# Kernel tuning notes

Hardware: AMD Instinct MI355X
Metric: run time of the kernel (lower is better)

The kernel has to match this reference:

```python
import jax, jax.numpy as jnp
import numpy as np

B, NDOC, L, E = 32, 4, 512, 512
SCALE = np.float32(1.0 / np.sqrt(E))
NEG_INF = np.float32(-1e9)


def setup_inputs() -> dict:
    key = jax.random.key(0)
    k1, k2, k3, k4, k5, k6 = jax.random.split(key, 6)
    return {
        "x1": jax.random.normal(k1, (B, L, E), dtype=jnp.float32),
        "x2": jax.random.normal(k2, (B, NDOC, L, E), dtype=jnp.float32),
        "x1_len": jax.random.randint(k3, (B,), 0, L, dtype=jnp.int64),
        "x2_len": jax.random.randint(k4, (B, NDOC), 0, L, dtype=jnp.int64),
        "fusion_w": jax.random.normal(k5, (2 * E, E), dtype=jnp.float32) * 0.02,
        "fusion_b": jnp.zeros((E,), dtype=jnp.float32),
        "out_w": jax.random.normal(k6, (8 * E, 2 * E), dtype=jnp.float32) * 0.02,
        "out_b": jnp.zeros((2 * E,), dtype=jnp.float32),
    }


def reference(x1, x2, x1_len, x2_len, fusion_w, fusion_b, out_w, out_b):
    # Faithful to torch .repeat(1,4,...): concatenate 4 full copies along batch,
    # so attention row i pairs x1[i % B] with x2[i // 4, i % 4].
    x1_rep = jnp.tile(x1, (NDOC, 1, 1))          # [4B, L, E]
    x2_r = x2.reshape(-1, L, E)                  # [4B, L, E]

    x1_len_r = jnp.tile(x1_len, NDOC)            # [4B] (same tiling as x1_rep)
    x2_len_r = x2_len.reshape(-1)                # [4B]
    pos = jnp.arange(L)
    q_mask = pos[None, :] < x1_len_r[:, None]    # [4B, L]
    k_mask = pos[None, :] < x2_len_r[:, None]    # [4B, L]
    mask = q_mask[:, :, None] & k_mask[:, None, :]  # [4B, L, L]

    # scaled-dot-product attention with masked_fill(mask==0, -1e9)
    scores = jnp.einsum('bqe,bke->bqk', x1_rep, x2_r) * SCALE  # [4B, L, L]
    scores = jnp.where(mask, scores, NEG_INF)
    attn = jax.nn.softmax(scores, axis=-1)
    x1_att = jnp.einsum('bqk,bke->bqe', attn, x2_r)            # [4B, L, E]

    cat = jnp.concatenate([x1_rep - x1_att, x1_rep * x1_att], axis=-1)  # [4B, L, 2E]
    fus = jax.nn.relu(cat @ fusion_w + fusion_b)                        # [4B, L, E]

    x1_mean = jnp.mean(fus, axis=1)              # [4B, E]
    x1_max = jnp.max(fus, axis=1)                # [4B, E]
    pooled = jnp.concatenate([x1_mean.reshape(B, -1), x1_max.reshape(B, -1)], axis=-1)  # [B, 8E]
    out = jax.nn.relu(pooled @ out_w + out_b)    # [B, 2E]
    return out, attn
```

## Files before the change

### kernel.cpp

```cpp
#include <hip/hip_runtime.h>
#include <cstddef>

#define BATCH 32
#define NB    128
#define LL    512
#define EE    512
#define SCALE 0.044194173824159216f
#define NEG_INF -1e9f

typedef __attribute__((ext_vector_type(4))) float f32x4;
typedef __attribute__((ext_vector_type(8))) short s16x8;
typedef __attribute__((ext_vector_type(4))) unsigned short u16x4;

__device__ __forceinline__ unsigned short f2b(float f) {
    unsigned u = __float_as_uint(f);
    u += 0x7FFFu + ((u >> 16) & 1u);
    return (unsigned short)(u >> 16);
}
__device__ __forceinline__ float b2f(unsigned short h) {
    return __uint_as_float(((unsigned)h) << 16);
}

__device__ __forceinline__ void gld_lds16(const unsigned short* g, unsigned short* l) {
    __builtin_amdgcn_global_load_lds(
        (const __attribute__((address_space(1))) void*)g,
        (__attribute__((address_space(3))) void*)l, 16, 0, 0);
}

__global__ __launch_bounds__(256) void k_cvt_x1(
    const float* __restrict__ x1, unsigned short* __restrict__ x1bf)
{
    const size_t idx = (size_t)blockIdx.x * 256 + threadIdx.x;
    f32x4 v = *(const f32x4*)(x1 + idx * 4);
    u16x4 o = { f2b(v[0]), f2b(v[1]), f2b(v[2]), f2b(v[3]) };
    *(u16x4*)(x1bf + idx * 4) = o;
}

__global__ __launch_bounds__(256) void k_cvt_x2(
    const float* __restrict__ x2,
    unsigned short* __restrict__ x2bf, unsigned short* __restrict__ x2t)
{
    __shared__ float T[64][65];
    const int i = blockIdx.z, kb = blockIdx.y * 64, eb = blockIdx.x * 64;
    const float* src = x2 + (size_t)i * LL * EE;
    unsigned short* db = x2bf + (size_t)i * LL * EE;
    unsigned short* dt = x2t  + (size_t)i * LL * EE;
    const int t = threadIdx.x, r16 = t >> 4, c4 = (t & 15) * 4;
#pragma unroll
    for (int p = 0; p < 4; ++p) {
        int row = p * 16 + r16;
        f32x4 v = *(const f32x4*)(src + (size_t)(kb + row) * EE + eb + c4);
        T[row][c4] = v[0]; T[row][c4+1] = v[1]; T[row][c4+2] = v[2]; T[row][c4+3] = v[3];
        u16x4 o = { f2b(v[0]), f2b(v[1]), f2b(v[2]), f2b(v[3]) };
        *(u16x4*)(db + (size_t)(kb + row) * EE + eb + c4) = o;
    }
    __syncthreads();
#pragma unroll
    for (int p = 0; p < 4; ++p) {
        int erow = p * 16 + r16;
        u16x4 o = { f2b(T[c4][erow]), f2b(T[c4+1][erow]),
                    f2b(T[c4+2][erow]), f2b(T[c4+3][erow]) };
        *(u16x4*)(dt + (size_t)(eb + erow) * LL + kb + c4) = o;
    }
}

__global__ __launch_bounds__(256) void k_cvt_fw(
    const float* __restrict__ fw, unsigned short* __restrict__ fwt)
{
    __shared__ float T[64][65];
    const int jb = blockIdx.y * 64, eb = blockIdx.x * 64;
    const int t = threadIdx.x, r16 = t >> 4, c4 = (t & 15) * 4;
#pragma unroll
    for (int p = 0; p < 4; ++p) {
        int row = p * 16 + r16;
        f32x4 v = *(const f32x4*)(fw + (size_t)(jb + row) * EE + eb + c4);
        T[row][c4] = v[0]; T[row][c4+1] = v[1]; T[row][c4+2] = v[2]; T[row][c4+3] = v[3];
    }
    __syncthreads();
#pragma unroll
    for (int p = 0; p < 4; ++p) {
        int erow = p * 16 + r16;
#pragma unroll
        for (int k = 0; k < 4; ++k) {
            int jold = jb + c4 + k;
            int jn = (jold < 512) ? (2 * jold) : (2 * (jold - 512) + 1);
            fwt[(size_t)(eb + erow) * 1024 + jn] = f2b(T[c4 + k][erow]);
        }
    }
}

__global__ __launch_bounds__(1024, 4) void k_attn(
    const unsigned short* __restrict__ x1bf,
    const unsigned short* __restrict__ x2bf,
    const unsigned short* __restrict__ x2t,
    const int* __restrict__ x1_len, const int* __restrict__ x2_len,
    float* __restrict__ attn, unsigned short* __restrict__ Cbuf)
{
    __shared__ __align__(16) char smem[147456];
    unsigned short* Ast = (unsigned short*)smem;
    unsigned short* Bst = (unsigned short*)(smem + 8192);
    unsigned short* Bpv = (unsigned short*)(smem + 131072);
    float* rowred = (float*)(smem + 131072);
    float* rowst  = (float*)(smem + 131072 + 4096);

    const int i  = blockIdx.x;
    const int q0 = blockIdx.y * 128;
    const unsigned short* Ag = x1bf + (size_t)(i & 31) * LL * EE;
    const unsigned short* Bg = x2bf + (size_t)i * LL * EE;
    const unsigned short* Vg = x2t  + (size_t)i * LL * EE;
    const int t = threadIdx.x, lane = t & 63;
    const int w = t >> 6;
    const int m = lane & 15, quad = lane >> 4;
    const int lrow = lane >> 2, lcol = (lane & 3) * 8;
    const int wrow = w >> 3, wcol = w & 7;

    f32x4 acc[4][4];
#pragma unroll
    for (int r = 0; r < 4; ++r)
#pragma unroll
        for (int c = 0; c < 4; ++c) acc[r][c] = (f32x4){0.f, 0.f, 0.f, 0.f};

    for (int e0 = 0; e0 < EE; e0 += 32) {
        if (w < 8)
            gld_lds16(Ag + (size_t)(q0 + w * 16 + lrow) * EE + e0 + lcol, &Ast[w * 512]);
        gld_lds16(Bg + (size_t)((2 * w) * 16 + lrow) * EE + e0 + lcol, &Bst[(2 * w) * 512]);
        gld_lds16(Bg + (size_t)((2 * w + 1) * 16 + lrow) * EE + e0 + lcol, &Bst[(2 * w + 1) * 512]);
        __syncthreads();
        s16x8 af[4], bfr[4];
#pragma unroll
        for (int rt = 0; rt < 4; ++rt)
            af[rt] = *(const s16x8*)&Ast[(wrow * 64 + rt * 16 + m) * 32 + quad * 8];
#pragma unroll
        for (int ct = 0; ct < 4; ++ct)
            bfr[ct] = *(const s16x8*)&Bst[(wcol * 64 + ct * 16 + m) * 32 + quad * 8];
#pragma unroll
        for (int rt = 0; rt < 4; ++rt)
#pragma unroll
            for (int ct = 0; ct < 4; ++ct)
                acc[rt][ct] = __builtin_amdgcn_mfma_f32_16x16x32_bf16(
                    af[rt], bfr[ct], acc[rt][ct], 0, 0, 0);
        __syncthreads();
    }

    const int qlen = x1_len[i & 31];
    const int klen = x2_len[i];

#pragma unroll
    for (int rt = 0; rt < 4; ++rt)
#pragma unroll
        for (int reg = 0; reg < 4; ++reg) {
            const int l = q0 + wrow * 64 + rt * 16 + quad * 4 + reg;
            const bool qok = l < qlen;
#pragma unroll
            for (int ct = 0; ct < 4; ++ct) {
                const int k = wcol * 64 + ct * 16 + m;
                acc[rt][ct][reg] = (qok && k < klen) ? acc[rt][ct][reg] * SCALE : NEG_INF;
            }
        }

#pragma unroll
    for (int rt = 0; rt < 4; ++rt)
#pragma unroll
        for (int reg = 0; reg < 4; ++reg) {
            float v = fmaxf(fmaxf(acc[rt][0][reg], acc[rt][1][reg]),
                            fmaxf(acc[rt][2][reg], acc[rt][3][reg]));
            v = fmaxf(v, __shfl_xor(v, 1));
            v = fmaxf(v, __shfl_xor(v, 2));
            v = fmaxf(v, __shfl_xor(v, 4));
            v = fmaxf(v, __shfl_xor(v, 8));
            if (m == 0)
                rowred[wcol * 128 + wrow * 64 + rt * 16 + quad * 4 + reg] = v;
        }
    __syncthreads();
    if (t < 128) {
        float mx = rowred[t];
#pragma unroll
        for (int c = 1; c < 8; ++c) mx = fmaxf(mx, rowred[c * 128 + t]);
        rowst[t] = mx;
    }
    __syncthreads();

#pragma unroll
    for (int rt = 0; rt < 4; ++rt)
#pragma unroll
        for (int reg = 0; reg < 4; ++reg) {
            const int lloc = wrow * 64 + rt * 16 + quad * 4 + reg;
            const float mx = rowst[lloc];
            float s = 0.f;
#pragma unroll
            for (int ct = 0; ct < 4; ++ct) {
                float p = __expf(acc[rt][ct][reg] - mx);
                acc[rt][ct][reg] = p;
                s += p;
            }
            s += __shfl_xor(s, 1);
            s += __shfl_xor(s, 2);
            s += __shfl_xor(s, 4);
            s += __shfl_xor(s, 8);
            if (m == 0) rowred[wcol * 128 + lloc] = s;
        }
    __syncthreads();
    if (t < 128) {
        float s = 0.f;
#pragma unroll
        for (int c = 0; c < 8; ++c) s += rowred[c * 128 + t];
        rowst[t] = 1.0f / s;
    }
    __syncthreads();

    float* op = attn + (size_t)i * LL * LL;
#pragma unroll
    for (int rt = 0; rt < 4; ++rt)
#pragma unroll
        for (int reg = 0; reg < 4; ++reg) {
            const int lloc = wrow * 64 + rt * 16 + quad * 4 + reg;
            const float inv = rowst[lloc];
#pragma unroll
            for (int ct = 0; ct < 4; ++ct) {
                const int k = wcol * 64 + ct * 16 + m;
                float p = acc[rt][ct][reg] * inv;
                op[(size_t)(q0 + lloc) * LL + k] = p;
                unsigned off = (unsigned)(lloc * 1024 + k * 2) ^ (unsigned)((lloc & 7) << 4);
                *(unsigned short*)(smem + off) = f2b(p);
            }
        }
    __syncthreads();

    const int pwr = w >> 2, pwc = w & 3;
    unsigned short* Cb = Cbuf + (size_t)i * LL * 1024;
#pragma unroll
    for (int eh = 0; eh < 2; ++eh) {
        f32x4 acc2[2][4];
#pragma unroll
        for (int r = 0; r < 2; ++r)
#pragma unroll
            for (int c = 0; c < 4; ++c) acc2[r][c] = (f32x4){0.f, 0.f, 0.f, 0.f};

        for (int k0 = 0; k0 < LL; k0 += 32) {
            gld_lds16(Vg + (size_t)(eh * 256 + w * 16 + lrow) * LL + k0 + lcol, &Bpv[w * 512]);
            __syncthreads();
            s16x8 paf[2], pbf[4];
#pragma unroll
            for (int rt = 0; rt < 2; ++rt) {
                const int lr = pwr * 32 + rt * 16 + m;
                unsigned off = (unsigned)(lr * 1024 + (k0 + quad * 8) * 2)
                               ^ (unsigned)((lr & 7) << 4);
                paf[rt] = *(const s16x8*)(smem + off);
            }
#pragma unroll
            for (int ct = 0; ct < 4; ++ct)
                pbf[ct] = *(const s16x8*)&Bpv[(pwc * 64 + ct * 16 + m) * 32 + quad * 8];
#pragma unroll
            for (int rt = 0; rt < 2; ++rt)
#pragma unroll
                for (int ct = 0; ct < 4; ++ct)
                    acc2[rt][ct] = __builtin_amdgcn_mfma_f32_16x16x32_bf16(
                        paf[rt], pbf[ct], acc2[rt][ct], 0, 0, 0);
            __syncthreads();
        }

#pragma unroll
        for (int rt = 0; rt < 2; ++rt)
#pragma unroll
            for (int reg = 0; reg < 4; ++reg) {
                const int l = q0 + pwr * 32 + rt * 16 + quad * 4 + reg;
#pragma unroll
                for (int ct = 0; ct < 4; ++ct) {
                    const int e = eh * 256 + pwc * 64 + ct * 16 + m;
                    float att = acc2[rt][ct][reg];
                    float xv  = b2f(Ag[(size_t)l * EE + e]);
                    unsigned pr = (unsigned)f2b(xv - att) | ((unsigned)f2b(xv * att) << 16);
                    *(unsigned*)(Cb + (size_t)l * 1024 + 2 * e) = pr;
                }
            }
    }
}

__global__ __launch_bounds__(256) void k_fuse_mfma(
    const unsigned short* __restrict__ Cbuf,
    const unsigned short* __restrict__ fwt,
    const float* __restrict__ fb,
    float* __restrict__ pmean, float* __restrict__ pmax)
{
    __shared__ unsigned short Al[128 * 32];
    __shared__ unsigned short Bl[128 * 32];
    __shared__ float psum[2][128];
    __shared__ float pmx[2][128];
    const int i  = blockIdx.x;
    const int lt = blockIdx.y >> 2;
    const int e0 = (blockIdx.y & 3) * 128;
    const unsigned short* Ab = Cbuf + ((size_t)i * LL + lt * 128) * 1024;
    const int t = threadIdx.x, lane = t & 63;
    const int w = t >> 6, wrow = w >> 1, wcol = w & 1;
    const int m = lane & 15, quad = lane >> 4;
    const int lrow = lane >> 2, lcol = (lane & 3) * 8;

    float bias[4];
#pragma unroll
    for (int ct = 0; ct < 4; ++ct) bias[ct] = fb[e0 + wcol * 64 + ct * 16 + m];
    float csum[4] = {0.f, 0.f, 0.f, 0.f};
    float cmax[4] = {-3e38f, -3e38f, -3e38f, -3e38f};

    f32x4 acc[4][4];
#pragma unroll
    for (int r = 0; r < 4; ++r)
#pragma unroll
        for (int c = 0; c < 4; ++c) acc[r][c] = (f32x4){0.f, 0.f, 0.f, 0.f};

    for (int j0 = 0; j0 < 1024; j0 += 32) {
#pragma unroll
        for (int c = 0; c < 2; ++c) {
            const int s = c * 4 + w;
            gld_lds16(Ab + (size_t)(s * 16 + lrow) * 1024 + j0 + lcol, &Al[s * 512]);
            gld_lds16(fwt + (size_t)(e0 + s * 16 + lrow) * 1024 + j0 + lcol, &Bl[s * 512]);
        }
        __syncthreads();
        s16x8 af[4], bfr[4];
#pragma unroll
        for (int rt = 0; rt < 4; ++rt)
            af[rt] = *(const s16x8*)&Al[(wrow * 64 + rt * 16 + m) * 32 + quad * 8];
#pragma unroll
        for (int ct = 0; ct < 4; ++ct)
            bfr[ct] = *(const s16x8*)&Bl[(wcol * 64 + ct * 16 + m) * 32 + quad * 8];
#pragma unroll
        for (int rt = 0; rt < 4; ++rt)
#pragma unroll
            for (int ct = 0; ct < 4; ++ct)
                acc[rt][ct] = __builtin_amdgcn_mfma_f32_16x16x32_bf16(
                    af[rt], bfr[ct], acc[rt][ct], 0, 0, 0);
        __syncthreads();
    }
#pragma unroll
    for (int rt = 0; rt < 4; ++rt)
#pragma unroll
        for (int reg = 0; reg < 4; ++reg)
#pragma unroll
            for (int ct = 0; ct < 4; ++ct) {
                float f = fmaxf(acc[rt][ct][reg] + bias[ct], 0.f);
                csum[ct] += f;
                cmax[ct] = fmaxf(cmax[ct], f);
            }
#pragma unroll
    for (int ct = 0; ct < 4; ++ct) {
        csum[ct] += __shfl_xor(csum[ct], 16);
        csum[ct] += __shfl_xor(csum[ct], 32);
        cmax[ct] = fmaxf(cmax[ct], __shfl_xor(cmax[ct], 16));
        cmax[ct] = fmaxf(cmax[ct], __shfl_xor(cmax[ct], 32));
    }
    if (quad == 0) {
#pragma unroll
        for (int ct = 0; ct < 4; ++ct) {
            psum[wrow][wcol * 64 + ct * 16 + m] = csum[ct];
            pmx[wrow][wcol * 64 + ct * 16 + m] = cmax[ct];
        }
    }
    __syncthreads();
    if (t < 128) {
        float s  = psum[0][t] + psum[1][t];
        float mx = fmaxf(pmx[0][t], pmx[1][t]);
        pmean[((size_t)i * 4 + lt) * EE + e0 + t] = s;
        pmax[((size_t)i * 4 + lt) * EE + e0 + t]  = mx;
    }
}

__global__ __launch_bounds__(256) void k_out_split(
    const float* __restrict__ pmean, const float* __restrict__ pmax,
    const float* __restrict__ ow, float* __restrict__ partial)
{
    __shared__ float ps[256];
    const int kc = blockIdx.x;
    const int b  = blockIdx.y;
    const int t  = threadIdx.x;
    const int j  = kc * 256 + t;
    const int jj = (j < 2048) ? j : j - 2048;
    const int ii = 4 * b + (jj >> 9);
    const int e  = jj & 511;
    float v;
    if (j < 2048) {
        const float* bp = pmean + (size_t)ii * 4 * EE + e;
        v = (bp[0] + bp[512] + bp[1024] + bp[1536]) * (1.0f / 512.0f);
    } else {
        const float* bp = pmax + (size_t)ii * 4 * EE + e;
        v = fmaxf(fmaxf(bp[0], bp[512]), fmaxf(bp[1024], bp[1536]));
    }
    ps[t] = v;
    __syncthreads();
    f32x4 acc = {0.f, 0.f, 0.f, 0.f};
    const float* wp = ow + (size_t)kc * 256 * 1024 + t * 4;
#pragma unroll 8
    for (int q = 0; q < 256; ++q) {
        f32x4 w4 = *(const f32x4*)(wp + (size_t)q * 1024);
        float p = ps[q];
        acc[0] = fmaf(p, w4[0], acc[0]);
        acc[1] = fmaf(p, w4[1], acc[1]);
        acc[2] = fmaf(p, w4[2], acc[2]);
        acc[3] = fmaf(p, w4[3], acc[3]);
    }
    *(f32x4*)(partial + ((size_t)kc * 32 + b) * 1024 + t * 4) = acc;
}

__global__ __launch_bounds__(256) void k_out_final(
    const float* __restrict__ partial, const float* __restrict__ ob,
    float* __restrict__ out)
{
    const int idx = blockIdx.x * 256 + threadIdx.x;
    const int b = idx >> 10, o = idx & 1023;
    float s = ob[o];
#pragma unroll
    for (int kc = 0; kc < 16; ++kc)
        s += partial[((size_t)kc * 32 + b) * 1024 + o];
    out[idx] = fmaxf(s, 0.f);
}

extern "C" void kernel_launch(void* const* d_in, const int* in_sizes, int n_in,
                              void* d_out, int out_size, void* d_ws, size_t ws_size,
                              hipStream_t stream)
{
    const float* x1     = (const float*)d_in[0];
    const float* x2     = (const float*)d_in[1];
    const int*   x1_len = (const int*)d_in[2];
    const int*   x2_len = (const int*)d_in[3];
    const float* fw     = (const float*)d_in[4];
    const float* fb     = (const float*)d_in[5];
    const float* ow     = (const float*)d_in[6];
    const float* ob     = (const float*)d_in[7];

    float* out  = (float*)d_out;
    float* attn = out + (size_t)BATCH * 1024;

    char* wp = (char*)d_ws;
    unsigned short* x1bf   = (unsigned short*)wp; wp += (size_t)BATCH * LL * EE * 2;
    unsigned short* x2bf   = (unsigned short*)wp; wp += (size_t)NB * LL * EE * 2;
    unsigned short* x2t    = (unsigned short*)wp; wp += (size_t)NB * LL * EE * 2;
    unsigned short* Cbuf   = (unsigned short*)wp; wp += (size_t)NB * LL * 1024 * 2;
    unsigned short* fwt    = (unsigned short*)wp; wp += (size_t)EE * 1024 * 2;
    float* pmean   = (float*)wp; wp += (size_t)NB * 4 * EE * 4;
    float* pmax    = (float*)wp; wp += (size_t)NB * 4 * EE * 4;
    float* partial = (float*)wp; wp += (size_t)16 * BATCH * 1024 * 4;

    k_cvt_x1<<<dim3(BATCH * LL * EE / 4 / 256), 256, 0, stream>>>(x1, x1bf);
    k_cvt_x2<<<dim3(8, 8, NB), 256, 0, stream>>>(x2, x2bf, x2t);
    k_cvt_fw<<<dim3(8, 16), 256, 0, stream>>>(fw, fwt);
    k_attn<<<dim3(128, 4), 1024, 0, stream>>>(x1bf, x2bf, x2t, x1_len, x2_len, attn, Cbuf);
    k_fuse_mfma<<<dim3(128, 16), 256, 0, stream>>>(Cbuf, fwt, fb, pmean, pmax);
    k_out_split<<<dim3(16, BATCH), 256, 0, stream>>>(pmean, pmax, ow, partial);
    k_out_final<<<dim3(BATCH * 1024 / 256), 256, 0, stream>>>(partial, ob, out);
}
```

Measured before the change: 578.5 us.

## Double-buffer LDS staging in attention and fusion GEMM loops

Adds ping-pong LDS buffers to the QK^T, PV and fusion GEMM main loops. Each loop prefetches the next 32-wide K slice while MFMAs run on the current one, and drops one barrier per iteration. The aim is to hide global-to-LDS load latency behind matrix math. The cost is that the attention kernel's shared memory grows to 160 KB, the full per-CU LDS, and the fusion kernel's LDS use doubles, which may reduce occupancy there.

```diff
diff --git a/kernel.cpp b/kernel.cpp
--- a/kernel.cpp
+++ b/kernel.cpp
@@ -96,10 +96,13 @@
     const int* __restrict__ x1_len, const int* __restrict__ x2_len,
     float* __restrict__ attn, unsigned short* __restrict__ Cbuf)
 {
-    __shared__ __align__(16) char smem[147456];
-    unsigned short* Ast = (unsigned short*)smem;
-    unsigned short* Bst = (unsigned short*)(smem + 8192);
-    unsigned short* Bpv = (unsigned short*)(smem + 131072);
+    __shared__ __align__(16) char smem[163840];
+    unsigned short* A0 = (unsigned short*)smem;
+    unsigned short* B0 = (unsigned short*)(smem + 8192);
+    unsigned short* A1 = (unsigned short*)(smem + 40960);
+    unsigned short* B1 = (unsigned short*)(smem + 49152);
+    unsigned short* V0 = (unsigned short*)(smem + 131072);
+    unsigned short* V1 = (unsigned short*)(smem + 147456);
     float* rowred = (float*)(smem + 131072);
     float* rowst  = (float*)(smem + 131072 + 4096);
 
@@ -120,19 +123,31 @@
 #pragma unroll
         for (int c = 0; c < 4; ++c) acc[r][c] = (f32x4){0.f, 0.f, 0.f, 0.f};
 
-    for (int e0 = 0; e0 < EE; e0 += 32) {
-        if (w < 8)
-            gld_lds16(Ag + (size_t)(q0 + w * 16 + lrow) * EE + e0 + lcol, &Ast[w * 512]);
-        gld_lds16(Bg + (size_t)((2 * w) * 16 + lrow) * EE + e0 + lcol, &Bst[(2 * w) * 512]);
-        gld_lds16(Bg + (size_t)((2 * w + 1) * 16 + lrow) * EE + e0 + lcol, &Bst[(2 * w + 1) * 512]);
-        __syncthreads();
+    if (w < 8)
+        gld_lds16(Ag + (size_t)(q0 + w * 16 + lrow) * EE + lcol, &A0[w * 512]);
+    gld_lds16(Bg + (size_t)((2 * w) * 16 + lrow) * EE + lcol, &B0[(2 * w) * 512]);
+    gld_lds16(Bg + (size_t)((2 * w + 1) * 16 + lrow) * EE + lcol, &B0[(2 * w + 1) * 512]);
+    __syncthreads();
+
+    for (int it = 0; it < 16; ++it) {
+        unsigned short* Ac = (it & 1) ? A1 : A0;
+        unsigned short* Bc = (it & 1) ? B1 : B0;
+        if (it < 15) {
+            unsigned short* An = (it & 1) ? A0 : A1;
+            unsigned short* Bn = (it & 1) ? B0 : B1;
+            const int e0n = (it + 1) * 32;
+            if (w < 8)
+                gld_lds16(Ag + (size_t)(q0 + w * 16 + lrow) * EE + e0n + lcol, &An[w * 512]);
+            gld_lds16(Bg + (size_t)((2 * w) * 16 + lrow) * EE + e0n + lcol, &Bn[(2 * w) * 512]);
+            gld_lds16(Bg + (size_t)((2 * w + 1) * 16 + lrow) * EE + e0n + lcol, &Bn[(2 * w + 1) * 512]);
+        }
         s16x8 af[4], bfr[4];
 #pragma unroll
         for (int rt = 0; rt < 4; ++rt)
-            af[rt] = *(const s16x8*)&Ast[(wrow * 64 + rt * 16 + m) * 32 + quad * 8];
+            af[rt] = *(const s16x8*)&Ac[(wrow * 64 + rt * 16 + m) * 32 + quad * 8];
 #pragma unroll
         for (int ct = 0; ct < 4; ++ct)
-            bfr[ct] = *(const s16x8*)&Bst[(wcol * 64 + ct * 16 + m) * 32 + quad * 8];
+            bfr[ct] = *(const s16x8*)&Bc[(wcol * 64 + ct * 16 + m) * 32 + quad * 8];
 #pragma unroll
         for (int rt = 0; rt < 4; ++rt)
 #pragma unroll
@@ -236,9 +251,17 @@
 #pragma unroll
             for (int c = 0; c < 4; ++c) acc2[r][c] = (f32x4){0.f, 0.f, 0.f, 0.f};
 
-        for (int k0 = 0; k0 < LL; k0 += 32) {
-            gld_lds16(Vg + (size_t)(eh * 256 + w * 16 + lrow) * LL + k0 + lcol, &Bpv[w * 512]);
-            __syncthreads();
+        gld_lds16(Vg + (size_t)(eh * 256 + w * 16 + lrow) * LL + lcol, &V0[w * 512]);
+        __syncthreads();
+
+        for (int kt = 0; kt < 16; ++kt) {
+            const int k0 = kt * 32;
+            unsigned short* Vc = (kt & 1) ? V1 : V0;
+            if (kt < 15) {
+                unsigned short* Vn = (kt & 1) ? V0 : V1;
+                gld_lds16(Vg + (size_t)(eh * 256 + w * 16 + lrow) * LL + k0 + 32 + lcol,
+                          &Vn[w * 512]);
+            }
             s16x8 paf[2], pbf[4];
 #pragma unroll
             for (int rt = 0; rt < 2; ++rt) {
@@ -249,7 +272,7 @@
             }
 #pragma unroll
             for (int ct = 0; ct < 4; ++ct)
-                pbf[ct] = *(const s16x8*)&Bpv[(pwc * 64 + ct * 16 + m) * 32 + quad * 8];
+                pbf[ct] = *(const s16x8*)&Vc[(pwc * 64 + ct * 16 + m) * 32 + quad * 8];
 #pragma unroll
             for (int rt = 0; rt < 2; ++rt)
 #pragma unroll
@@ -282,8 +305,8 @@
     const float* __restrict__ fb,
     float* __restrict__ pmean, float* __restrict__ pmax)
 {
-    __shared__ unsigned short Al[128 * 32];
-    __shared__ unsigned short Bl[128 * 32];
+    __shared__ unsigned short Al[2][128 * 32];
+    __shared__ unsigned short Bl[2][128 * 32];
     __shared__ float psum[2][128];
     __shared__ float pmx[2][128];
     const int i  = blockIdx.x;
@@ -307,21 +330,34 @@
 #pragma unroll
         for (int c = 0; c < 4; ++c) acc[r][c] = (f32x4){0.f, 0.f, 0.f, 0.f};
 
-    for (int j0 = 0; j0 < 1024; j0 += 32) {
-#pragma unroll
-        for (int c = 0; c < 2; ++c) {
-            const int s = c * 4 + w;
-            gld_lds16(Ab + (size_t)(s * 16 + lrow) * 1024 + j0 + lcol, &Al[s * 512]);
-            gld_lds16(fwt + (size_t)(e0 + s * 16 + lrow) * 1024 + j0 + lcol, &Bl[s * 512]);
-        }
-        __syncthreads();
+#pragma unroll
+    for (int c = 0; c < 2; ++c) {
+        const int s = c * 4 + w;
+        gld_lds16(Ab + (size_t)(s * 16 + lrow) * 1024 + lcol, &Al[0][s * 512]);
+        gld_lds16(fwt + (size_t)(e0 + s * 16 + lrow) * 1024 + lcol, &Bl[0][s * 512]);
+    }
+    __syncthreads();
+
+    for (int it = 0; it < 32; ++it) {
+        const int cur = it & 1;
+        if (it < 31) {
+            const int j0n = (it + 1) * 32;
+#pragma unroll
+            for (int c = 0; c < 2; ++c) {
+                const int s = c * 4 + w;
+                gld_lds16(Ab + (size_t)(s * 16 + lrow) * 1024 + j0n + lcol,
+                          &Al[cur ^ 1][s * 512]);
+                gld_lds16(fwt + (size_t)(e0 + s * 16 + lrow) * 1024 + j0n + lcol,
+                          &Bl[cur ^ 1][s * 512]);
+            }
+        }
         s16x8 af[4], bfr[4];
 #pragma unroll
         for (int rt = 0; rt < 4; ++rt)
-            af[rt] = *(const s16x8*)&Al[(wrow * 64 + rt * 16 + m) * 32 + quad * 8];
+            af[rt] = *(const s16x8*)&Al[cur][(wrow * 64 + rt * 16 + m) * 32 + quad * 8];
 #pragma unroll
         for (int ct = 0; ct < 4; ++ct)
-            bfr[ct] = *(const s16x8*)&Bl[(wcol * 64 + ct * 16 + m) * 32 + quad * 8];
+            bfr[ct] = *(const s16x8*)&Bl[cur][(wcol * 64 + ct * 16 + m) * 32 + quad * 8];
 #pragma unroll
         for (int rt = 0; rt < 4; ++rt)
 #pragma unroll
```

After: 582.0 us. About the same (+0.6%).

## Double-buffer LDS tiles in QK and PV loops and remap blocks per XCD

Applied to the files above, without the earlier changes.

The QK^T and PV main loops now use ping-pong LDS buffers: the next K-slice is issued via global_load_lds before the MFMAs on the current slice run, with one waitcnt+barrier per step instead of two __syncthreads. The block index is also remapped so the four query tiles of the same batch row land on the same XCD, which should improve L2 reuse of x2. LDS use rises to 160KB and the explicit vmcnt(0) fence still serialises at each step's end, so the overlap is limited to one MFMA step.

```diff
diff --git a/kernel.cpp b/kernel.cpp
--- a/kernel.cpp
+++ b/kernel.cpp
@@ -12,6 +12,8 @@
 typedef __attribute__((ext_vector_type(8))) short s16x8;
 typedef __attribute__((ext_vector_type(4))) unsigned short u16x4;
 
+#define STEP_FENCE() asm volatile("s_waitcnt vmcnt(0) lgkmcnt(0)\n\ts_barrier" ::: "memory")
+
 __device__ __forceinline__ unsigned short f2b(float f) {
     unsigned u = __float_as_uint(f);
     u += 0x7FFFu + ((u >> 16) & 1u);
@@ -96,15 +98,21 @@
     const int* __restrict__ x1_len, const int* __restrict__ x2_len,
     float* __restrict__ attn, unsigned short* __restrict__ Cbuf)
 {
-    __shared__ __align__(16) char smem[147456];
-    unsigned short* Ast = (unsigned short*)smem;
-    unsigned short* Bst = (unsigned short*)(smem + 8192);
-    unsigned short* Bpv = (unsigned short*)(smem + 131072);
+    __shared__ __align__(16) char smem[163840];
+    unsigned short* Ast0 = (unsigned short*)smem;
+    unsigned short* Ast1 = (unsigned short*)(smem + 8192);
+    unsigned short* Bst0 = (unsigned short*)(smem + 16384);
+    unsigned short* Bst1 = (unsigned short*)(smem + 49152);
     float* rowred = (float*)(smem + 131072);
     float* rowst  = (float*)(smem + 131072 + 4096);
-
-    const int i  = blockIdx.x;
-    const int q0 = blockIdx.y * 128;
+    unsigned short* Vst0 = (unsigned short*)(smem + 131072);
+    unsigned short* Vst1 = (unsigned short*)(smem + 147456);
+
+    const int flat = blockIdx.x + blockIdx.y * 128;
+    const int xcd  = flat & 7;
+    const int idx  = flat >> 3;
+    const int i    = xcd * 16 + (idx >> 2);
+    const int q0   = (idx & 3) * 128;
     const unsigned short* Ag = x1bf + (size_t)(i & 31) * LL * EE;
     const unsigned short* Bg = x2bf + (size_t)i * LL * EE;
     const unsigned short* Vg = x2t  + (size_t)i * LL * EE;
@@ -120,26 +128,38 @@
 #pragma unroll
         for (int c = 0; c < 4; ++c) acc[r][c] = (f32x4){0.f, 0.f, 0.f, 0.f};
 
-    for (int e0 = 0; e0 < EE; e0 += 32) {
-        if (w < 8)
-            gld_lds16(Ag + (size_t)(q0 + w * 16 + lrow) * EE + e0 + lcol, &Ast[w * 512]);
-        gld_lds16(Bg + (size_t)((2 * w) * 16 + lrow) * EE + e0 + lcol, &Bst[(2 * w) * 512]);
-        gld_lds16(Bg + (size_t)((2 * w + 1) * 16 + lrow) * EE + e0 + lcol, &Bst[(2 * w + 1) * 512]);
-        __syncthreads();
+    if (w < 8)
+        gld_lds16(Ag + (size_t)(q0 + w * 16 + lrow) * EE + lcol, &Ast0[w * 512]);
+    gld_lds16(Bg + (size_t)((2 * w) * 16 + lrow) * EE + lcol, &Bst0[(2 * w) * 512]);
+    gld_lds16(Bg + (size_t)((2 * w + 1) * 16 + lrow) * EE + lcol, &Bst0[(2 * w + 1) * 512]);
+    STEP_FENCE();
+
+    for (int it = 0; it < 16; ++it) {
+        unsigned short* Ac = (it & 1) ? Ast1 : Ast0;
+        unsigned short* Bc = (it & 1) ? Bst1 : Bst0;
+        if (it < 15) {
+            unsigned short* An = (it & 1) ? Ast0 : Ast1;
+            unsigned short* Bn = (it & 1) ? Bst0 : Bst1;
+            const int e0n = (it + 1) * 32;
+            if (w < 8)
+                gld_lds16(Ag + (size_t)(q0 + w * 16 + lrow) * EE + e0n + lcol, &An[w * 512]);
+            gld_lds16(Bg + (size_t)((2 * w) * 16 + lrow) * EE + e0n + lcol, &Bn[(2 * w) * 512]);
+            gld_lds16(Bg + (size_t)((2 * w + 1) * 16 + lrow) * EE + e0n + lcol, &Bn[(2 * w + 1) * 512]);
+        }
         s16x8 af[4], bfr[4];
 #pragma unroll
         for (int rt = 0; rt < 4; ++rt)
-            af[rt] = *(const s16x8*)&Ast[(wrow * 64 + rt * 16 + m) * 32 + quad * 8];
+            af[rt] = *(const s16x8*)&Ac[(wrow * 64 + rt * 16 + m) * 32 + quad * 8];
 #pragma unroll
         for (int ct = 0; ct < 4; ++ct)
-            bfr[ct] = *(const s16x8*)&Bst[(wcol * 64 + ct * 16 + m) * 32 + quad * 8];
+            bfr[ct] = *(const s16x8*)&Bc[(wcol * 64 + ct * 16 + m) * 32 + quad * 8];
 #pragma unroll
         for (int rt = 0; rt < 4; ++rt)
 #pragma unroll
             for (int ct = 0; ct < 4; ++ct)
                 acc[rt][ct] = __builtin_amdgcn_mfma_f32_16x16x32_bf16(
                     af[rt], bfr[ct], acc[rt][ct], 0, 0, 0);
-        __syncthreads();
+        STEP_FENCE();
     }
 
     const int qlen = x1_len[i & 31];
@@ -236,9 +256,17 @@
 #pragma unroll
             for (int c = 0; c < 4; ++c) acc2[r][c] = (f32x4){0.f, 0.f, 0.f, 0.f};
 
-        for (int k0 = 0; k0 < LL; k0 += 32) {
-            gld_lds16(Vg + (size_t)(eh * 256 + w * 16 + lrow) * LL + k0 + lcol, &Bpv[w * 512]);
-            __syncthreads();
+        gld_lds16(Vg + (size_t)(eh * 256 + w * 16 + lrow) * LL + lcol, &Vst0[w * 512]);
+        STEP_FENCE();
+
+        for (int kt = 0; kt < 16; ++kt) {
+            const int k0 = kt * 32;
+            unsigned short* Vc = (kt & 1) ? Vst1 : Vst0;
+            if (kt < 15) {
+                unsigned short* Vn = (kt & 1) ? Vst0 : Vst1;
+                gld_lds16(Vg + (size_t)(eh * 256 + w * 16 + lrow) * LL + k0 + 32 + lcol,
+                          &Vn[w * 512]);
+            }
             s16x8 paf[2], pbf[4];
 #pragma unroll
             for (int rt = 0; rt < 2; ++rt) {
@@ -249,14 +277,14 @@
             }
 #pragma unroll
             for (int ct = 0; ct < 4; ++ct)
-                pbf[ct] = *(const s16x8*)&Bpv[(pwc * 64 + ct * 16 + m) * 32 + quad * 8];
+                pbf[ct] = *(const s16x8*)&Vc[(pwc * 64 + ct * 16 + m) * 32 + quad * 8];
 #pragma unroll
             for (int rt = 0; rt < 2; ++rt)
 #pragma unroll
                 for (int ct = 0; ct < 4; ++ct)
                     acc2[rt][ct] = __builtin_amdgcn_mfma_f32_16x16x32_bf16(
                         paf[rt], pbf[ct], acc2[rt][ct], 0, 0, 0);
-            __syncthreads();
+            STEP_FENCE();
         }
 
 #pragma unroll
```

After: 576.7 us. Within noise of the previous version (-0.3%).
